# Performance work log

Hardware: AMD Instinct MI355X
Metric: run time of the kernel (lower is better)

Reference implementation:

```python
import jax, jax.numpy as jnp
import numpy as np


def _make_grid(h, w, stride=1):
    """Vectorized port of gen_grid_coordinates_exp. Returns (1, 3*Ho, 3*Wo, 2) float32,
    last dim = (x_norm, y_norm) in [-1,1] (torch grid_sample convention)."""
    rows = np.arange(0, h, stride)
    cols = np.arange(0, w, stride)
    theta = -((rows + 0.5) / h * np.pi - np.pi / 2)          # (Ho,)
    phi = (cols + 0.5) / w * 2 * np.pi - np.pi               # (Wo,)
    dtheta = np.pi / h
    dphi = 2 * np.pi / w
    # 3x3 tangent-plane offsets (du: horizontal, dv: vertical), per get_exp_duv
    du = np.tan(dphi) * np.array([[-1., 0., 1.]] * 3)                      # (3,3)
    dv = np.tan(dtheta) * np.array([[1., 1., 1.], [0., 0., 0.], [-1., -1., -1.]])
    T = theta[:, None, None, None]   # (Ho,1,1,1)
    P = phi[None, :, None, None]     # (1,Wo,1,1)
    u_x = -du * np.sin(P) - dv * np.sin(T) * np.cos(P)       # (Ho,Wo,3,3)
    u_y = du * np.cos(P) - dv * np.sin(T) * np.sin(P)
    u_z = dv * np.cos(T) + np.zeros_like(u_x)
    u_norm = np.sqrt(u_x ** 2 + u_y ** 2 + u_z ** 2)
    u_div = np.where(u_norm == 0, 1.0, u_norm)
    c, s = np.cos(u_norm), np.sin(u_norm)
    ex = np.cos(T) * np.cos(P) * c + u_x / u_div * s
    ey = np.cos(T) * np.sin(P) * c + u_y / u_div * s
    ez = np.sin(T) * c + u_z / u_div * s
    new_phi = np.arctan2(ey, ex)
    new_theta = np.arcsin(np.clip(ez, -1.0, 1.0))
    new_r = (-new_theta + np.pi / 2) * h / np.pi - 0.5
    new_c = ((new_phi + np.pi) * w / (2 * np.pi) - 0.5 + w) % w
    # kernel center samples the original integer pixel exactly
    new_r[:, :, 1, 1] = rows[:, None]
    new_c[:, :, 1, 1] = cols[None, :]
    gx = new_c * 2.0 / w - 1.0
    gy = new_r * 2.0 / h - 1.0
    grid = np.stack([gx, gy], axis=-1)                        # (Ho,Wo,3,3,2)
    Ho, Wo = len(rows), len(cols)
    grid = grid.transpose(0, 2, 1, 3, 4).reshape(1, Ho * 3, Wo * 3, 2)
    return grid.astype(np.float32)


def _grid_sample_bilinear(x, grid):
    """torch.nn.functional.grid_sample(mode='bilinear', padding='zeros', align_corners=False).
    x: (B,C,H,W); grid: (1,Hg,Wg,2) shared across batch."""
    B, C, H, W = x.shape
    gx = grid[0, ..., 0]
    gy = grid[0, ..., 1]
    Hg, Wg = gx.shape
    ix = ((gx + 1.0) * W - 1.0) * 0.5   # unnormalize, align_corners=False
    iy = ((gy + 1.0) * H - 1.0) * 0.5
    x0 = jnp.floor(ix); x1 = x0 + 1.0
    y0 = jnp.floor(iy); y1 = y0 + 1.0
    xf = x.reshape(B, C, H * W)

    def corner(xc, yc, wgt):
        valid = (xc >= 0) & (xc < W) & (yc >= 0) & (yc < H)
        xi = jnp.clip(xc, 0, W - 1).astype(jnp.int32)
        yi = jnp.clip(yc, 0, H - 1).astype(jnp.int32)
        idx = (yi * W + xi).reshape(-1)                      # (Hg*Wg,)
        w_eff = (wgt * valid.astype(wgt.dtype)).reshape(-1)  # zero-pad OOB
        return xf[:, :, idx] * w_eff                          # (B,C,Hg*Wg)

    out = (corner(x0, y0, (x1 - ix) * (y1 - iy))
           + corner(x1, y0, (ix - x0) * (y1 - iy))
           + corner(x0, y1, (x1 - ix) * (iy - y0))
           + corner(x1, y1, (ix - x0) * (iy - y0)))
    return out.reshape(B, C, Hg, Wg)


def setup_inputs() -> dict:
    key = jax.random.key(0)
    k1, k2 = jax.random.split(key)
    B, Cin, Cout, H, W = 4, 128, 256, 128, 256
    x = jax.random.normal(k1, (B, Cin, H, W), dtype=jnp.float32)
    # kaiming_uniform_(a=sqrt(5)) -> U(-1/sqrt(fan_in), 1/sqrt(fan_in)), fan_in = Cin*9
    bound = 1.0 / np.sqrt(Cin * 9)
    weight = jax.random.uniform(k2, (Cout, Cin, 3, 3), dtype=jnp.float32,
                                minval=-bound, maxval=bound)
    bias = jnp.zeros((Cout,), dtype=jnp.float32)
    grid = jnp.asarray(_make_grid(H, W, stride=1))  # (1, 3H, 3W, 2)
    return {"x": x, "weight": weight, "bias": bias, "grid": grid}


def reference(x, weight, bias, grid):
    sampled = _grid_sample_bilinear(x, grid)                 # (B,C,3H,3W)
    out = jax.lax.conv_general_dilated(
        sampled, weight, window_strides=(3, 3), padding='VALID',
        dimension_numbers=('NCHW', 'OIHW', 'NCHW'))          # (B,Cout,H,W)
    return out + bias[None, :, None, None]
```

## Files before the change

### kernel.cpp

```cpp
#include <hip/hip_runtime.h>


#define Hh   128
#define Ww   256
#define HWp  (Hh*Ww)
#define CIN  128
#define COUT 256
#define KTOT 1152
#define NPTS (384*768)
#define BM   64
#define BN   256
#define BK   32
#define NKS  (KTOT/BK)

typedef __attribute__((ext_vector_type(8))) _Float16 f16x8;
typedef __attribute__((ext_vector_type(4))) float    f32x4;

__device__ __forceinline__ f16x8 bcast8(float f) {
    _Float16 h = (_Float16)f;
    f16x8 v;
#pragma unroll
    for (int i = 0; i < 8; ++i) v[i] = h;
    return v;
}

__global__ void prep(const float* __restrict__ grid, const float* __restrict__ w,
                     const float* __restrict__ x,
                     int2* __restrict__ tI, float4* __restrict__ tW,
                     _Float16* __restrict__ wt2, _Float16* __restrict__ xt) {
    const int bid = blockIdx.x;
    const int t   = threadIdx.x;
    if (bid < NPTS / 256) {
        int g = bid * 256 + t;
        int hh = g / 768, ww = g - hh * 768;
        int ho = hh / 3, ii = hh - 3 * ho;
        int wo = ww / 3, jj = ww - 3 * wo;

        float gx = grid[2 * g + 0];
        float gy = grid[2 * g + 1];
        float ix = ((gx + 1.0f) * (float)Ww - 1.0f) * 0.5f;
        float iy = ((gy + 1.0f) * (float)Hh - 1.0f) * 0.5f;
        float x0f = floorf(ix), y0f = floorf(iy);
        int x0 = (int)x0f, y0 = (int)y0f;
        float wx1 = ix - x0f, wx0 = 1.0f - wx1;
        float wy1 = iy - y0f, wy0 = 1.0f - wy1;

        float wyt = (y0 >= 0 && y0 < Hh) ? wy0 : 0.0f;
        float wyb = (y0 + 1 >= 0 && y0 + 1 < Hh) ? wy1 : 0.0f;
        int r0 = min(max(y0, 0), Hh - 1);
        int r1 = min(max(y0 + 1, 0), Hh - 1);

        int xb; float cw0, cw1;
        if (x0 < 0)            { xb = 0;      cw0 = wx1; cw1 = 0.0f; }
        else if (x0 > Ww - 2)  { xb = Ww - 2; cw0 = 0.0f; cw1 = wx0; }
        else                   { xb = x0;     cw0 = wx0; cw1 = wx1; }

        int e = (ho * Ww + wo) * 9 + ii * 3 + jj;
        tI[e] = make_int2(r0 * Ww + xb, r1 * Ww + xb);
        tW[e] = make_float4(cw0 * wyt, cw1 * wyt, cw0 * wyb, cw1 * wyb);
    } else if (bid < 2 * (NPTS / 256)) {
        int o = (bid - NPTS / 256) * 256 + t;
        int kk = o & (BK - 1);
        int n  = (o >> 5) & (COUT - 1);
        int ks = o >> 13;
        int ij = ks % 9;
        int ci = (ks / 9) * 32 + kk;
        wt2[o] = (_Float16)w[n * KTOT + ci * 9 + ij];
    } else {
        int r  = (bid - 2 * (NPTS / 256)) * 256 + t;
        int sp = r & (HWp - 1);
        int cg = (r >> 15) & 15;
        int b  = r >> 19;
        const float* src = x + ((size_t)(b * CIN + cg * 8)) * HWp + sp;
        f16x8 v;
#pragma unroll
        for (int j = 0; j < 8; ++j) v[j] = (_Float16)src[(size_t)j * HWp];
        *(f16x8*)&xt[((size_t)(b * HWp + sp)) * CIN + cg * 8] = v;
    }
}

__global__ __launch_bounds__(512, 4) void sphconv_gemm(
    const _Float16* __restrict__ xt, const _Float16* __restrict__ wt2,
    const float* __restrict__ bias, const int2* __restrict__ tI,
    const float4* __restrict__ tW, float* __restrict__ out) {

    __shared__ int2   sTI[9 * BM];
    __shared__ float4 sTW[9 * BM];
    __shared__ __align__(16) _Float16 sA[2][BM * 40];
    __shared__ __align__(16) _Float16 sB[2][BN * 40];

    const int t = threadIdx.x;
    const int bid = blockIdx.x;
    const int swz = (bid & 7) * 256 + (bid >> 3);
    const int m0  = swz * BM;
    const int b   = m0 >> 15;
    const int sp0 = m0 & (HWp - 1);
    const _Float16* xb_ = xt + (size_t)b * (HWp * CIN);

    for (int e = t; e < 9 * BM; e += 512) {
        int r = e & (BM - 1), ij = e >> 6;
        sTI[e] = tI[(sp0 + r) * 9 + ij];
        sTW[e] = tW[(sp0 + r) * 9 + ij];
    }

    const int lane = t & 63;
    const int wid  = t >> 6;
    const int wrow = wid >> 2;
    const int wcol = wid & 3;
    const int quad = lane >> 4;
    const int l16  = lane & 15;

    const bool isA = (t < 256);
    const int  mr  = t & 63;
    const int  chb = ((t >> 6) & 3) * 8;
    const int  u   = t - 256;

    f32x4 acc[2][4];
#pragma unroll
    for (int r = 0; r < 2; ++r)
#pragma unroll
        for (int c = 0; c < 4; ++c) {
            f32x4 z = {0.0f, 0.0f, 0.0f, 0.0f};
            acc[r][c] = z;
        }

    __syncthreads();

    f16x8 p00, p01, p10, p11;
    float4 wv;
    f16x8 b0v, b1v, b2v, b3v;
    if (isA) {
        const int2 o = sTI[mr];
        wv = sTW[mr];
        const _Float16* p = xb_ + (size_t)o.x * CIN + chb;
        const _Float16* q = xb_ + (size_t)o.y * CIN + chb;
        p00 = *(const f16x8*)p;  p01 = *(const f16x8*)(p + CIN);
        p10 = *(const f16x8*)q;  p11 = *(const f16x8*)(q + CIN);
        f16x8 av = p00 * bcast8(wv.x) + p01 * bcast8(wv.y)
                 + p10 * bcast8(wv.z) + p11 * bcast8(wv.w);
        *(f16x8*)&sA[0][mr * 40 + chb] = av;
    } else {
        const _Float16* src = wt2 + u * BK;
        b0v = *(const f16x8*)(src);      b1v = *(const f16x8*)(src + 8);
        b2v = *(const f16x8*)(src + 16); b3v = *(const f16x8*)(src + 24);
        *(f16x8*)&sB[0][u * 40 + 0]  = b0v;
        *(f16x8*)&sB[0][u * 40 + 8]  = b1v;
        *(f16x8*)&sB[0][u * 40 + 16] = b2v;
        *(f16x8*)&sB[0][u * 40 + 24] = b3v;
    }
    __syncthreads();

    int ij = 0, cb = 0;
    for (int ks = 0; ks < NKS; ++ks) {
        const int cur = ks & 1, nxt = cur ^ 1;
        const bool have = (ks + 1 < NKS);
        const int ij2 = (ij == 8) ? 0 : ij + 1;
        const int cb2 = (ij == 8) ? cb + 32 : cb;

        if (have) {
            if (isA) {
                const int2 o = sTI[ij2 * BM + mr];
                wv = sTW[ij2 * BM + mr];
                const _Float16* p = xb_ + (size_t)o.x * CIN + cb2 + chb;
                const _Float16* q = xb_ + (size_t)o.y * CIN + cb2 + chb;
                p00 = *(const f16x8*)p;  p01 = *(const f16x8*)(p + CIN);
                p10 = *(const f16x8*)q;  p11 = *(const f16x8*)(q + CIN);
            } else {
                const _Float16* src = wt2 + (size_t)(ks + 1) * (COUT * BK) + u * BK;
                b0v = *(const f16x8*)(src);      b1v = *(const f16x8*)(src + 8);
                b2v = *(const f16x8*)(src + 16); b3v = *(const f16x8*)(src + 24);
            }
        }

        f16x8 af[2], bfr[4];
#pragma unroll
        for (int r = 0; r < 2; ++r)
            af[r] = *(const f16x8*)(&sA[cur][(wrow * 32 + r * 16 + l16) * 40 + quad * 8]);
#pragma unroll
        for (int c = 0; c < 4; ++c)
            bfr[c] = *(const f16x8*)(&sB[cur][(wcol * 64 + c * 16 + l16) * 40 + quad * 8]);
#pragma unroll
        for (int r = 0; r < 2; ++r)
#pragma unroll
            for (int c = 0; c < 4; ++c)
                acc[r][c] = __builtin_amdgcn_mfma_f32_16x16x32_f16(
                    af[r], bfr[c], acc[r][c], 0, 0, 0);

        if (have) {
            if (isA) {
                f16x8 av = p00 * bcast8(wv.x) + p01 * bcast8(wv.y)
                         + p10 * bcast8(wv.z) + p11 * bcast8(wv.w);
                *(f16x8*)&sA[nxt][mr * 40 + chb] = av;
            } else {
                *(f16x8*)&sB[nxt][u * 40 + 0]  = b0v;
                *(f16x8*)&sB[nxt][u * 40 + 8]  = b1v;
                *(f16x8*)&sB[nxt][u * 40 + 16] = b2v;
                *(f16x8*)&sB[nxt][u * 40 + 24] = b3v;
            }
        }

        __syncthreads();
        ij = ij2; cb = cb2;
    }

#pragma unroll
    for (int c = 0; c < 4; ++c) {
        int n = wcol * 64 + c * 16 + l16;
        float bv = bias[n];
        float* outn = out + (((size_t)(b * COUT + n)) << 15) + sp0;
#pragma unroll
        for (int r = 0; r < 2; ++r) {
            int mbase = wrow * 32 + r * 16 + quad * 4;
            float4 v = make_float4(acc[r][c][0] + bv, acc[r][c][1] + bv,
                                   acc[r][c][2] + bv, acc[r][c][3] + bv);
            *(float4*)(&outn[mbase]) = v;
        }
    }
}

extern "C" void kernel_launch(void* const* d_in, const int* in_sizes, int n_in,
                              void* d_out, int out_size, void* d_ws, size_t ws_size,
                              hipStream_t stream) {
    const float* x    = (const float*)d_in[0];
    const float* w    = (const float*)d_in[1];
    const float* bias = (const float*)d_in[2];
    const float* grid = (const float*)d_in[3];
    float* out = (float*)d_out;

    char* ws = (char*)d_ws;
    int2*     tI  = (int2*)(ws);
    float4*   tW  = (float4*)(ws + 2359296);
    _Float16* wt2 = (_Float16*)(ws + 7077888);
    _Float16* xt  = (_Float16*)(ws + 7667712);

    prep<<<1152 + 1152 + 8192, 256, 0, stream>>>(grid, w, x, tI, tW, wt2, xt);
    sphconv_gemm<<<(4 * HWp) / BM, 512, 0, stream>>>(xt, wt2, bias, tI, tW, out);
}
```

Measured before the change: 416.5 us.

## Load B fragments directly from global and vectorize x transpose

Each wave in the GEMM kernel now loads its weight fragments straight from global memory into registers, double-buffered across an unrolled pair of k-steps. This removes the shared-memory B tile and its staging stores. The prep transpose now reads float4 per channel and writes four spatial positions per thread, so it launches fewer blocks. The trade is more redundant global/L2 traffic for weights, since every block rereads them, and more register pressure.

```diff
diff --git a/kernel.cpp b/kernel.cpp
--- a/kernel.cpp
+++ b/kernel.cpp
@@ -67,15 +67,21 @@
         int ci = (ks / 9) * 32 + kk;
         wt2[o] = (_Float16)w[n * KTOT + ci * 9 + ij];
     } else {
-        int r  = (bid - 2 * (NPTS / 256)) * 256 + t;
-        int sp = r & (HWp - 1);
-        int cg = (r >> 15) & 15;
-        int b  = r >> 19;
-        const float* src = x + ((size_t)(b * CIN + cg * 8)) * HWp + sp;
-        f16x8 v;
-#pragma unroll
-        for (int j = 0; j < 8; ++j) v[j] = (_Float16)src[(size_t)j * HWp];
-        *(f16x8*)&xt[((size_t)(b * HWp + sp)) * CIN + cg * 8] = v;
+        int r   = (bid - 2 * (NPTS / 256)) * 256 + t;
+        int sp4 = (r & 8191) * 4;
+        int cg  = (r >> 13) & 15;
+        int b   = r >> 17;
+        const float* src = x + ((size_t)(b * CIN + cg * 8)) * HWp + sp4;
+        float4 v[8];
+#pragma unroll
+        for (int j = 0; j < 8; ++j) v[j] = *(const float4*)(src + (size_t)j * HWp);
+#pragma unroll
+        for (int s = 0; s < 4; ++s) {
+            f16x8 ov;
+#pragma unroll
+            for (int j = 0; j < 8; ++j) ov[j] = (_Float16)((&v[j].x)[s]);
+            *(f16x8*)&xt[((size_t)(b * HWp + sp4 + s)) * CIN + cg * 8] = ov;
+        }
     }
 }
 
@@ -87,7 +93,6 @@
     __shared__ int2   sTI[9 * BM];
     __shared__ float4 sTW[9 * BM];
     __shared__ __align__(16) _Float16 sA[2][BM * 40];
-    __shared__ __align__(16) _Float16 sB[2][BN * 40];
 
     const int t = threadIdx.x;
     const int bid = blockIdx.x;
@@ -113,7 +118,8 @@
     const bool isA = (t < 256);
     const int  mr  = t & 63;
     const int  chb = ((t >> 6) & 3) * 8;
-    const int  u   = t - 256;
+
+    const _Float16* wfrag = wt2 + (wcol * 64 + l16) * BK + quad * 8;
 
     f32x4 acc[2][4];
 #pragma unroll
@@ -126,82 +132,69 @@
 
     __syncthreads();
 
-    f16x8 p00, p01, p10, p11;
-    float4 wv;
-    f16x8 b0v, b1v, b2v, b3v;
+    f16x8 bc[4], bn[4];
     if (isA) {
-        const int2 o = sTI[mr];
-        wv = sTW[mr];
+        const int2   o  = sTI[mr];
+        const float4 wv = sTW[mr];
         const _Float16* p = xb_ + (size_t)o.x * CIN + chb;
         const _Float16* q = xb_ + (size_t)o.y * CIN + chb;
-        p00 = *(const f16x8*)p;  p01 = *(const f16x8*)(p + CIN);
-        p10 = *(const f16x8*)q;  p11 = *(const f16x8*)(q + CIN);
-        f16x8 av = p00 * bcast8(wv.x) + p01 * bcast8(wv.y)
-                 + p10 * bcast8(wv.z) + p11 * bcast8(wv.w);
+        f16x8 av = (*(const f16x8*)p)         * bcast8(wv.x)
+                 + (*(const f16x8*)(p + CIN)) * bcast8(wv.y)
+                 + (*(const f16x8*)q)         * bcast8(wv.z)
+                 + (*(const f16x8*)(q + CIN)) * bcast8(wv.w);
         *(f16x8*)&sA[0][mr * 40 + chb] = av;
-    } else {
-        const _Float16* src = wt2 + u * BK;
-        b0v = *(const f16x8*)(src);      b1v = *(const f16x8*)(src + 8);
-        b2v = *(const f16x8*)(src + 16); b3v = *(const f16x8*)(src + 24);
-        *(f16x8*)&sB[0][u * 40 + 0]  = b0v;
-        *(f16x8*)&sB[0][u * 40 + 8]  = b1v;
-        *(f16x8*)&sB[0][u * 40 + 16] = b2v;
-        *(f16x8*)&sB[0][u * 40 + 24] = b3v;
-    }
+    }
+#pragma unroll
+    for (int c = 0; c < 4; ++c)
+        bc[c] = *(const f16x8*)(wfrag + c * 16 * BK);
     __syncthreads();
 
-    int ij = 0, cb = 0;
-    for (int ks = 0; ks < NKS; ++ks) {
-        const int cur = ks & 1, nxt = cur ^ 1;
-        const bool have = (ks + 1 < NKS);
-        const int ij2 = (ij == 8) ? 0 : ij + 1;
-        const int cb2 = (ij == 8) ? cb + 32 : cb;
-
-        if (have) {
-            if (isA) {
-                const int2 o = sTI[ij2 * BM + mr];
-                wv = sTW[ij2 * BM + mr];
-                const _Float16* p = xb_ + (size_t)o.x * CIN + cb2 + chb;
-                const _Float16* q = xb_ + (size_t)o.y * CIN + cb2 + chb;
-                p00 = *(const f16x8*)p;  p01 = *(const f16x8*)(p + CIN);
-                p10 = *(const f16x8*)q;  p11 = *(const f16x8*)(q + CIN);
-            } else {
-                const _Float16* src = wt2 + (size_t)(ks + 1) * (COUT * BK) + u * BK;
-                b0v = *(const f16x8*)(src);      b1v = *(const f16x8*)(src + 8);
-                b2v = *(const f16x8*)(src + 16); b3v = *(const f16x8*)(src + 24);
-            }
-        }
-
-        f16x8 af[2], bfr[4];
-#pragma unroll
-        for (int r = 0; r < 2; ++r)
-            af[r] = *(const f16x8*)(&sA[cur][(wrow * 32 + r * 16 + l16) * 40 + quad * 8]);
-#pragma unroll
-        for (int c = 0; c < 4; ++c)
-            bfr[c] = *(const f16x8*)(&sB[cur][(wcol * 64 + c * 16 + l16) * 40 + quad * 8]);
-#pragma unroll
-        for (int r = 0; r < 2; ++r)
-#pragma unroll
-            for (int c = 0; c < 4; ++c)
-                acc[r][c] = __builtin_amdgcn_mfma_f32_16x16x32_f16(
-                    af[r], bfr[c], acc[r][c], 0, 0, 0);
-
-        if (have) {
-            if (isA) {
-                f16x8 av = p00 * bcast8(wv.x) + p01 * bcast8(wv.y)
-                         + p10 * bcast8(wv.z) + p11 * bcast8(wv.w);
-                *(f16x8*)&sA[nxt][mr * 40 + chb] = av;
-            } else {
-                *(f16x8*)&sB[nxt][u * 40 + 0]  = b0v;
-                *(f16x8*)&sB[nxt][u * 40 + 8]  = b1v;
-                *(f16x8*)&sB[nxt][u * 40 + 16] = b2v;
-                *(f16x8*)&sB[nxt][u * 40 + 24] = b3v;
-            }
-        }
-
-        __syncthreads();
-        ij = ij2; cb = cb2;
-    }
+#define STEP_BODY(KS, CURA, NXTA, BCUR, BNXT)                                   \
+    {                                                                           \
+        const int  ks_   = (KS);                                                \
+        const bool have_ = (ks_ + 1 < NKS);                                     \
+        f16x8 p00, p01, p10, p11;                                               \
+        float4 wv;                                                              \
+        if (isA && have_) {                                                     \
+            const int ij2 = (ks_ + 1) % 9;                                      \
+            const int cb2 = ((ks_ + 1) / 9) * 32;                               \
+            const int2 o = sTI[ij2 * BM + mr];                                  \
+            wv = sTW[ij2 * BM + mr];                                            \
+            const _Float16* p = xb_ + (size_t)o.x * CIN + cb2 + chb;            \
+            const _Float16* q = xb_ + (size_t)o.y * CIN + cb2 + chb;            \
+            p00 = *(const f16x8*)p;  p01 = *(const f16x8*)(p + CIN);            \
+            p10 = *(const f16x8*)q;  p11 = *(const f16x8*)(q + CIN);            \
+        }                                                                       \
+        if (have_) {                                                            \
+            const _Float16* src = wfrag + (size_t)(ks_ + 1) * (COUT * BK);      \
+            _Pragma("unroll")                                                   \
+            for (int c = 0; c < 4; ++c)                                         \
+                BNXT[c] = *(const f16x8*)(src + c * 16 * BK);                   \
+        }                                                                       \
+        f16x8 af[2];                                                            \
+        _Pragma("unroll")                                                       \
+        for (int r = 0; r < 2; ++r)                                             \
+            af[r] = *(const f16x8*)(&CURA[(wrow * 32 + r * 16 + l16) * 40 +     \
+                                          quad * 8]);                           \
+        _Pragma("unroll")                                                       \
+        for (int r = 0; r < 2; ++r)                                             \
+            _Pragma("unroll")                                                   \
+            for (int c = 0; c < 4; ++c)                                         \
+                acc[r][c] = __builtin_amdgcn_mfma_f32_16x16x32_f16(             \
+                    af[r], BCUR[c], acc[r][c], 0, 0, 0);                        \
+        if (isA && have_) {                                                     \
+            f16x8 av = p00 * bcast8(wv.x) + p01 * bcast8(wv.y)                  \
+                     + p10 * bcast8(wv.z) + p11 * bcast8(wv.w);                 \
+            *(f16x8*)&NXTA[mr * 40 + chb] = av;                                 \
+        }                                                                       \
+        __syncthreads();                                                        \
+    }
+
+    for (int ks = 0; ks < NKS; ks += 2) {
+        STEP_BODY(ks,     sA[0], sA[1], bc, bn)
+        STEP_BODY(ks + 1, sA[1], sA[0], bn, bc)
+    }
+#undef STEP_BODY
 
 #pragma unroll
     for (int c = 0; c < 4; ++c) {
@@ -233,6 +226,6 @@
     _Float16* wt2 = (_Float16*)(ws + 7077888);
     _Float16* xt  = (_Float16*)(ws + 7667712);
 
-    prep<<<1152 + 1152 + 8192, 256, 0, stream>>>(grid, w, x, tI, tW, wt2, xt);
+    prep<<<1152 + 1152 + 2048, 256, 0, stream>>>(grid, w, x, tI, tW, wt2, xt);
     sphconv_gemm<<<(4 * HWp) / BM, 512, 0, stream>>>(xt, wt2, bias, tI, tW, out);
 }
```

Result: slower. 485.6 us (+16.6%).
